# Kernel optimization log

Hardware: AMD Instinct MI355X
Metric: run time of the kernel (lower is better)

The kernel has to match this reference:

```python
import jax, jax.numpy as jnp
import numpy as np

N = 100_000       # nodes
E = 1_600_000     # edges (avg degree 16)
HID = 128         # hidden_size
NH = 8            # num_attention_heads
HD = HID // NH    # attention_head_size = 16


def setup_inputs() -> dict:
    key = jax.random.key(0)
    ks = jax.random.split(key, 9)
    s = 1.0 / np.sqrt(HID)
    h = jax.random.normal(ks[0], (N, HID), jnp.float32)
    src = jax.random.randint(ks[1], (E,), 0, N, dtype=jnp.int32)
    dst = jax.random.randint(ks[2], (E,), 0, N, dtype=jnp.int32)
    Wq = jax.random.normal(ks[3], (HID, HID), jnp.float32) * s
    Wk = jax.random.normal(ks[4], (HID, HID), jnp.float32) * s
    Wv = jax.random.normal(ks[5], (HID, HID), jnp.float32) * s
    bq = jnp.zeros((HID,), jnp.float32)
    bk = jnp.zeros((HID,), jnp.float32)
    bv = jnp.zeros((HID,), jnp.float32)
    return {"h": h, "src": src, "dst": dst,
            "Wq": Wq, "bq": bq, "Wk": Wk, "bk": bk, "Wv": Wv, "bv": bv}


def reference(h, src, dst, Wq, bq, Wk, bk, Wv, bv):
    # Linear projections, split heads: [N, NH, HD]
    Q = (h @ Wq + bq).reshape(N, NH, HD)
    K = (h @ Wk + bk).reshape(N, NH, HD)
    V = (h @ Wv + bv).reshape(N, NH, HD)

    # per-edge score: sum_d K[src] * Q[dst]  (no 1/sqrt(d) scaling in original)
    score = jnp.sum(K[src] * Q[dst], axis=-1)            # [E, NH]

    # edge_softmax: segment softmax over edges sharing the same destination
    m = jax.ops.segment_max(score, dst, num_segments=N)  # [N, NH]
    p = jnp.exp(score - m[dst])                          # [E, NH]
    denom = jax.ops.segment_sum(p, dst, num_segments=N)  # [N, NH]
    p = p / denom[dst]

    # (dropout prob = 0.0 -> identity)
    # message = V[src] * attn_probs; reduce = scatter-sum at destination
    msg = V[src] * p[:, :, None]                         # [E, NH, HD]
    out = jax.ops.segment_sum(msg, dst, num_segments=N)  # [N, NH, HD]
    return out.reshape(N, NH * HD)
```

## Files before the change

kernel.cpp:

```cpp
#include <hip/hip_runtime.h>
#include <stdint.h>

typedef unsigned short u16;
typedef u16      u16x8 __attribute__((ext_vector_type(8)));
typedef _Float16 f16x8 __attribute__((ext_vector_type(8)));
typedef float    f32x4 __attribute__((ext_vector_type(4)));
typedef unsigned long long u64;

#define HIDDEN 128
#define BSH    9
#define NPB    (1 << BSH)
#define MAXBUK 256
#define PAD    16


__device__ __forceinline__ float h2f(u16 u) {
    _Float16 h; __builtin_memcpy(&h, &u, 2); return (float)h;
}
__device__ __forceinline__ u16 f2h(float f) {
    _Float16 h = (_Float16)f; u16 u; __builtin_memcpy(&u, &h, 2); return u;
}
__device__ __forceinline__ float lo16f(uint32_t u) { return h2f((u16)(u & 0xffff)); }
__device__ __forceinline__ float hi16f(uint32_t u) { return h2f((u16)(u >> 16)); }

template <int CTRL>
__device__ __forceinline__ float dpp_qperm(float x) {
#if __has_builtin(__builtin_amdgcn_update_dpp)
    int r = __builtin_amdgcn_update_dpp(0, __builtin_bit_cast(int, x), CTRL, 0xF, 0xF, true);
    return __builtin_bit_cast(float, r);
#else
    return __shfl_xor(x, (CTRL == 0xB1) ? 1 : 2);
#endif
}

__global__ void pack_w_kernel(const float* __restrict__ Wq, const float* __restrict__ Wk,
                              const float* __restrict__ Wv, u16* __restrict__ packed) {
    int tid = blockIdx.x * blockDim.x + threadIdx.x;
    if (tid >= 24 * 4 * 64 * 8) return;
    int j    = tid & 7;
    int lane = (tid >> 3) & 63;
    int kt   = (tid >> 9) & 3;
    int ct   = tid >> 11;
    int w    = ct >> 3;
    int k    = kt * 32 + ((lane >> 4) << 3) + j;
    int c    = (ct & 7) * 16 + (lane & 15);
    const float* W = (w == 0) ? Wq : (w == 1) ? Wk : Wv;
    packed[tid] = f2h(W[k * HIDDEN + c]);
}

__global__ __launch_bounds__(256) void qkv_gemm_mfma(
    const float* __restrict__ h, const u16* __restrict__ packed,
    const float* __restrict__ bq, const float* __restrict__ bk, const float* __restrict__ bv,
    u16* __restrict__ Qb, u16* __restrict__ KVb, int n) {
    int wave = threadIdx.x >> 6, lane = threadIdx.x & 63;
    int row0 = blockIdx.x * 64 + wave * 16;
    int m = lane & 15, quad = lane >> 4;
    int arow = row0 + m;

    u16x8 a[4];
    if (arow < n) {
        const float* hp = h + (size_t)arow * HIDDEN + quad * 8;
        #pragma unroll
        for (int kt = 0; kt < 4; ++kt) {
            f32x4 lo = *(const f32x4*)(hp + kt * 32);
            f32x4 hi = *(const f32x4*)(hp + kt * 32 + 4);
            #pragma unroll
            for (int j = 0; j < 4; ++j) {
                a[kt][j]     = f2h(lo[j]);
                a[kt][j + 4] = f2h(hi[j]);
            }
        }
    } else {
        #pragma unroll
        for (int kt = 0; kt < 4; ++kt) a[kt] = (u16x8){0,0,0,0,0,0,0,0};
    }

    #pragma unroll
    for (int ct = 0; ct < 24; ++ct) {
        f32x4 acc = {0.f, 0.f, 0.f, 0.f};
        #pragma unroll
        for (int kt = 0; kt < 4; ++kt) {
            u16x8 b = *(const u16x8*)(packed + (((ct * 4 + kt) * 64 + lane) << 3));
            acc = __builtin_amdgcn_mfma_f32_16x16x32_f16(
                __builtin_bit_cast(f16x8, a[kt]), __builtin_bit_cast(f16x8, b),
                acc, 0, 0, 0);
        }
        int w  = ct >> 3;
        int cc = (ct & 7) * 16 + m;
        const float* bp = (w == 0) ? bq : (w == 1) ? bk : bv;
        float bias = bp[cc];
        #pragma unroll
        for (int r = 0; r < 4; ++r) {
            int rr = row0 + quad * 4 + r;
            if (rr < n) {
                u16 val = f2h(acc[r] + bias);
                if (w == 0) {
                    Qb[(size_t)rr * HIDDEN + cc] = val;
                } else {
                    KVb[(size_t)rr * 256 + ((cc >> 2) << 3) + ((w == 2) ? 4 : 0) + (cc & 3)] = val;
                }
            }
        }
    }
}

__global__ __launch_bounds__(256) void bucket_hist(const int* __restrict__ dst,
                                                   int* __restrict__ totalsPad,
                                                   int e, int nbuk) {
    __shared__ int lh[MAXBUK];
    int t = threadIdx.x;
    lh[t] = 0;
    __syncthreads();
    int stride = gridDim.x * blockDim.x;
    for (int i = blockIdx.x * blockDim.x + t; i < e; i += stride) {
        int b = dst[i] >> BSH;
        if (b < 0) b = 0; if (b >= nbuk) b = nbuk - 1;
        atomicAdd(&lh[b], 1);
    }
    __syncthreads();
    if (t < nbuk && lh[t] > 0) atomicAdd(&totalsPad[t * PAD], lh[t]);
}

__global__ __launch_bounds__(256) void bucket_scan(const int* __restrict__ totalsPad,
                                                   int* __restrict__ bs,
                                                   int* __restrict__ cursorPad,
                                                   int nbuk, int e) {
    __shared__ int buf[256];
    int t = threadIdx.x;
    int v = (t < nbuk) ? totalsPad[t * PAD] : 0;
    buf[t] = v;
    __syncthreads();
    #pragma unroll
    for (int off = 1; off < 256; off <<= 1) {
        int x = (t >= off) ? buf[t - off] : 0;
        __syncthreads();
        buf[t] += x;
        __syncthreads();
    }
    int excl = buf[t] - v;
    if (t < nbuk) {
        bs[t] = excl;
        cursorPad[t * PAD] = excl;
    }
    if (t == 0) bs[nbuk] = e;
}

__global__ __launch_bounds__(256) void bucket_scatter(
    const int* __restrict__ src, const int* __restrict__ dst,
    int* __restrict__ cursorPad, u64* __restrict__ pairs,
    int e, int nbuk, int chunk) {
    __shared__ int lh[MAXBUK];
    __shared__ int lcur[MAXBUK];
    int t = threadIdx.x;
    int lo = blockIdx.x * chunk;
    int hi = lo + chunk; if (hi > e) hi = e;
    if (lo >= e) return;
    lh[t] = 0;
    __syncthreads();
    for (int i = lo + t; i < hi; i += 256) {
        int b = dst[i] >> BSH;
        if (b < 0) b = 0; if (b >= nbuk) b = nbuk - 1;
        atomicAdd(&lh[b], 1);
    }
    __syncthreads();
    if (t < nbuk) {
        int c = lh[t];
        lcur[t] = (c > 0) ? atomicAdd(&cursorPad[t * PAD], c) : 0;
    }
    __syncthreads();
    for (int i = lo + t; i < hi; i += 256) {
        int d = dst[i], s = src[i];
        int b = d >> BSH;
        if (b < 0) b = 0; if (b >= nbuk) b = nbuk - 1;
        int slot = atomicAdd(&lcur[b], 1);
        if (slot >= 0 && slot < e)
            pairs[slot] = (((u64)(unsigned)d) << 32) | (unsigned)(s);
    }
}

__global__ __launch_bounds__(1024) void csr_finalize(
    const u64* __restrict__ pairs, const int* __restrict__ bs,
    int* __restrict__ starts, int* __restrict__ srcperm, int n, int e, int nbuk) {
    __shared__ int hist[NPB];
    __shared__ int excl[NPB];
    __shared__ int lcur[NPB];
    int b = blockIdx.x;
    int t = threadIdx.x;
    int d0 = b << BSH;
    int lo = bs[b], hi = bs[b + 1];
    for (int i = t; i < NPB; i += 1024) { hist[i] = 0; lcur[i] = 0; }
    __syncthreads();
    for (int i = lo + t; i < hi; i += 1024) {
        int ld = (int)(pairs[i] >> 32) - d0;
        if (ld < 0) ld = 0; if (ld >= NPB) ld = NPB - 1;
        atomicAdd(&hist[ld], 1);
    }
    __syncthreads();
    if (t < NPB) excl[t] = hist[t];
    __syncthreads();
    #pragma unroll
    for (int off = 1; off < NPB; off <<= 1) {
        int x = 0;
        if (t < NPB && t >= off) x = excl[t - off];
        __syncthreads();
        if (t < NPB) excl[t] += x;
        __syncthreads();
    }
    if (t < NPB) excl[t] -= hist[t];
    __syncthreads();
    if (t < NPB) {
        int d = d0 + t;
        if (d < n) starts[d] = lo + excl[t];
    }
    if (b == nbuk - 1 && t == 0) starts[n] = e;
    for (int i = lo + t; i < hi; i += 1024) {
        u64 p = pairs[i];
        int d  = (int)(p >> 32);
        int s  = (int)(p & 0xffffffffu);
        int ld = d - d0;
        if (ld < 0) ld = 0; if (ld >= NPB) ld = NPB - 1;
        int r = atomicAdd(&lcur[ld], 1);
        int slot = lo + excl[ld] + r;
        if (slot >= 0 && slot < e) srcperm[slot] = s;
    }
}

__global__ __launch_bounds__(256) void attn_kernel(
    const u16* __restrict__ Qb, const uint4* __restrict__ KVb,
    const int* __restrict__ starts, const int* __restrict__ srcperm,
    float* __restrict__ out, int n, int e) {
    int node = blockIdx.x * 4 + (threadIdx.x >> 6);
    int lane = threadIdx.x & 63;
    if (node >= n) return;
    int j = lane & 31;
    int h = lane >> 5;

    uint2 qp = *(const uint2*)(Qb + (size_t)node * HIDDEN + j * 4);
    float q0 = lo16f(qp.x), q1 = hi16f(qp.x);
    float q2 = lo16f(qp.y), q3 = hi16f(qp.y);

    int off = starts[node];
    int deg = starts[node + 1] - off;
    if (deg < 0) deg = 0; if (deg > e) deg = e;
    if (off < 0) off = 0; if (off > e - deg) off = e - deg;

    float mrun = -1e30f, lrun = 0.f;
    float o0 = 0.f, o1 = 0.f, o2 = 0.f, o3 = 0.f;

    for (int base = 0; base < deg; base += 64) {
        int cnt = deg - base; if (cnt > 64) cnt = 64;
        int sv = 0;
        if (lane < cnt) {
            int s = srcperm[off + base + lane];
            if (s < 0) s = 0; if (s >= n) s = n - 1;
            sv = s;
        }
        uint4 kvA = KVb[(size_t)__shfl(sv, h) * 32 + j];
        uint4 kvB = KVb[(size_t)__shfl(sv, 2 + h) * 32 + j];
        for (int i = 0; i < cnt; i += 2) {
            uint4 kv = kvA;
            kvA = kvB;
            int ip = i + 4 + h; if (ip > 63) ip = 63;
            kvB = KVb[(size_t)__shfl(sv, ip) * 32 + j];

            float p = q0 * lo16f(kv.x) + q1 * hi16f(kv.x)
                    + q2 * lo16f(kv.y) + q3 * hi16f(kv.y);
            p += dpp_qperm<0xB1>(p);
            p += dpp_qperm<0x4E>(p);
            bool valid = (i + h) < cnt;
            float pv = valid ? p : -1e30f;
            float mn  = fmaxf(mrun, pv);
            float scl = __expf(mrun - mn);
            float w   = valid ? __expf(pv - mn) : 0.f;
            lrun = lrun * scl + w;
            o0 = o0 * scl + w * lo16f(kv.z);
            o1 = o1 * scl + w * hi16f(kv.z);
            o2 = o2 * scl + w * lo16f(kv.w);
            o3 = o3 * scl + w * hi16f(kv.w);
            mrun = mn;
        }
    }

    float mo  = __shfl_xor(mrun, 32);
    float lo_ = __shfl_xor(lrun, 32);
    float p0 = __shfl_xor(o0, 32), p1 = __shfl_xor(o1, 32);
    float p2 = __shfl_xor(o2, 32), p3 = __shfl_xor(o3, 32);
    float m2 = fmaxf(mrun, mo);
    float sa = __expf(mrun - m2), sb = __expf(mo - m2);
    float l  = lrun * sa + lo_ * sb;
    float inv = (l > 0.f) ? 1.f / l : 0.f;
    if (h == 0) {
        float4 r;
        r.x = (o0 * sa + p0 * sb) * inv;
        r.y = (o1 * sa + p1 * sb) * inv;
        r.z = (o2 * sa + p2 * sb) * inv;
        r.w = (o3 * sa + p3 * sb) * inv;
        *(float4*)(out + (size_t)node * HIDDEN + j * 4) = r;
    }
}

extern "C" void kernel_launch(void* const* d_in, const int* in_sizes, int n_in,
                              void* d_out, int out_size, void* d_ws, size_t ws_size,
                              hipStream_t stream) {
    const float* h   = (const float*)d_in[0];
    const int*   src = (const int*)d_in[1];
    const int*   dst = (const int*)d_in[2];
    const float* Wq  = (const float*)d_in[3];
    const float* bq  = (const float*)d_in[4];
    const float* Wk  = (const float*)d_in[5];
    const float* bk  = (const float*)d_in[6];
    const float* Wv  = (const float*)d_in[7];
    const float* bv  = (const float*)d_in[8];
    float* out = (float*)d_out;

    const int n = in_sizes[0] / HIDDEN;
    const int e = in_sizes[1];
    const int nbuk = (n + NPB - 1) >> BSH;

    char* ws = (char*)d_ws;
    auto align256 = [](size_t x) { return (x + 255) & ~(size_t)255; };
    int* starts    = (int*)ws; ws += align256((size_t)(n + 1) * 4);
    int* bs        = (int*)ws; ws += align256((size_t)(MAXBUK + 1) * 4);
    int* totalsPad = (int*)ws; ws += align256((size_t)MAXBUK * PAD * 4);
    int* cursorPad = (int*)ws; ws += align256((size_t)MAXBUK * PAD * 4);
    int* srcperm   = (int*)ws; ws += align256((size_t)e * 4);
    u16* packed    = (u16*)ws; ws += align256((size_t)24 * 4 * 64 * 8 * sizeof(u16));
    u16* Qb        = (u16*)ws; ws += align256((size_t)n * HIDDEN * sizeof(u16));
    u16* KVb       = (u16*)ws; ws += align256((size_t)n * 256 * sizeof(u16));

    u64* pairs = (u64*)d_out;

    hipMemsetAsync(totalsPad, 0, (size_t)MAXBUK * PAD * 4, stream);

    pack_w_kernel<<<(24 * 4 * 64 * 8 + 255) / 256, 256, 0, stream>>>(Wq, Wk, Wv, packed);
    qkv_gemm_mfma<<<(n + 63) / 64, 256, 0, stream>>>(h, packed, bq, bk, bv, Qb, KVb, n);

    bucket_hist<<<256, 256, 0, stream>>>(dst, totalsPad, e, nbuk);
    bucket_scan<<<1, 256, 0, stream>>>(totalsPad, bs, cursorPad, nbuk, e);
    const int chunk = (e + 255) / 256;
    bucket_scatter<<<256, 256, 0, stream>>>(src, dst, cursorPad, pairs, e, nbuk, chunk);
    csr_finalize<<<nbuk, 1024, 0, stream>>>(pairs, bs, starts, srcperm, n, e, nbuk);

    attn_kernel<<<(n + 3) / 4, 256, 0, stream>>>(Qb, (const uint4*)KVb, starts, srcperm,
                                                 out, n, e);
}
```

Measured before the change: 331.4 us.

## Pack edge pairs into 32 bits, use fdot2/exp2, and prefetch indices directly

```diff
diff --git a/kernel.cpp b/kernel.cpp
--- a/kernel.cpp
+++ b/kernel.cpp
@@ -2,8 +2,10 @@
 #include <stdint.h>
 
 typedef unsigned short u16;
+typedef uint32_t u32;
 typedef u16      u16x8 __attribute__((ext_vector_type(8)));
 typedef _Float16 f16x8 __attribute__((ext_vector_type(8)));
+typedef _Float16 f16x2 __attribute__((ext_vector_type(2)));
 typedef float    f32x4 __attribute__((ext_vector_type(4)));
 typedef unsigned long long u64;
 
@@ -20,8 +22,9 @@
 __device__ __forceinline__ u16 f2h(float f) {
     _Float16 h = (_Float16)f; u16 u; __builtin_memcpy(&u, &h, 2); return u;
 }
-__device__ __forceinline__ float lo16f(uint32_t u) { return h2f((u16)(u & 0xffff)); }
-__device__ __forceinline__ float hi16f(uint32_t u) { return h2f((u16)(u >> 16)); }
+__device__ __forceinline__ f16x2 as_h2(uint32_t u) {
+    return __builtin_bit_cast(f16x2, u);
+}
 
 template <int CTRL>
 __device__ __forceinline__ float dpp_qperm(float x) {
@@ -30,6 +33,22 @@
     return __builtin_bit_cast(float, r);
 #else
     return __shfl_xor(x, (CTRL == 0xB1) ? 1 : 2);
+#endif
+}
+
+__device__ __forceinline__ float fdot2(f16x2 a, f16x2 b, float c) {
+#if __has_builtin(__builtin_amdgcn_fdot2)
+    return __builtin_amdgcn_fdot2(a, b, c, false);
+#else
+    return c + (float)a.x * (float)b.x + (float)a.y * (float)b.y;
+#endif
+}
+
+__device__ __forceinline__ float exp2f_fast(float x) {
+#if __has_builtin(__builtin_amdgcn_exp2f)
+    return __builtin_amdgcn_exp2f(x);
+#else
+    return __expf(x * 0.6931471805599453f);
 #endif
 }
 
@@ -147,7 +166,7 @@
 
 __global__ __launch_bounds__(256) void bucket_scatter(
     const int* __restrict__ src, const int* __restrict__ dst,
-    int* __restrict__ cursorPad, u64* __restrict__ pairs,
+    int* __restrict__ cursorPad, u32* __restrict__ pairs,
     int e, int nbuk, int chunk) {
     __shared__ int lh[MAXBUK];
     __shared__ int lcur[MAXBUK];
@@ -174,12 +193,12 @@
         if (b < 0) b = 0; if (b >= nbuk) b = nbuk - 1;
         int slot = atomicAdd(&lcur[b], 1);
         if (slot >= 0 && slot < e)
-            pairs[slot] = (((u64)(unsigned)d) << 32) | (unsigned)(s);
+            pairs[slot] = (((u32)d & (NPB - 1)) << 17) | ((u32)s & 0x1FFFF);
     }
 }
 
 __global__ __launch_bounds__(1024) void csr_finalize(
-    const u64* __restrict__ pairs, const int* __restrict__ bs,
+    const u32* __restrict__ pairs, const int* __restrict__ bs,
     int* __restrict__ starts, int* __restrict__ srcperm, int n, int e, int nbuk) {
     __shared__ int hist[NPB];
     __shared__ int excl[NPB];
@@ -191,8 +210,7 @@
     for (int i = t; i < NPB; i += 1024) { hist[i] = 0; lcur[i] = 0; }
     __syncthreads();
     for (int i = lo + t; i < hi; i += 1024) {
-        int ld = (int)(pairs[i] >> 32) - d0;
-        if (ld < 0) ld = 0; if (ld >= NPB) ld = NPB - 1;
+        int ld = (int)(pairs[i] >> 17);
         atomicAdd(&hist[ld], 1);
     }
     __syncthreads();
@@ -214,11 +232,9 @@
     }
     if (b == nbuk - 1 && t == 0) starts[n] = e;
     for (int i = lo + t; i < hi; i += 1024) {
-        u64 p = pairs[i];
-        int d  = (int)(p >> 32);
-        int s  = (int)(p & 0xffffffffu);
-        int ld = d - d0;
-        if (ld < 0) ld = 0; if (ld >= NPB) ld = NPB - 1;
+        u32 p = pairs[i];
+        int ld = (int)(p >> 17);
+        int s  = (int)(p & 0x1FFFF);
         int r = atomicAdd(&lcur[ld], 1);
         int slot = lo + excl[ld] + r;
         if (slot >= 0 && slot < e) srcperm[slot] = s;
@@ -236,49 +252,56 @@
     int h = lane >> 5;
 
     uint2 qp = *(const uint2*)(Qb + (size_t)node * HIDDEN + j * 4);
-    float q0 = lo16f(qp.x), q1 = hi16f(qp.x);
-    float q2 = lo16f(qp.y), q3 = hi16f(qp.y);
+    f16x2 q01 = as_h2(qp.x), q23 = as_h2(qp.y);
 
     int off = starts[node];
     int deg = starts[node + 1] - off;
     if (deg < 0) deg = 0; if (deg > e) deg = e;
     if (off < 0) off = 0; if (off > e - deg) off = e - deg;
 
+    const float LOG2E = 1.44269504f;
     float mrun = -1e30f, lrun = 0.f;
     float o0 = 0.f, o1 = 0.f, o2 = 0.f, o3 = 0.f;
 
-    for (int base = 0; base < deg; base += 64) {
-        int cnt = deg - base; if (cnt > 64) cnt = 64;
-        int sv = 0;
-        if (lane < cnt) {
-            int s = srcperm[off + base + lane];
-            if (s < 0) s = 0; if (s >= n) s = n - 1;
-            sv = s;
-        }
-        uint4 kvA = KVb[(size_t)__shfl(sv, h) * 32 + j];
-        uint4 kvB = KVb[(size_t)__shfl(sv, 2 + h) * 32 + j];
-        for (int i = 0; i < cnt; i += 2) {
+    if (deg > 0) {
+        const int last = deg - 1;
+        const int* sp = srcperm + off;
+        #define IDX(ii) (sp[((ii) > last) ? last : (ii)])
+        #define KVL(s)  (KVb[(size_t)(((unsigned)(s) < (unsigned)n) ? (unsigned)(s) : 0u) * 32 + j])
+
+        int sA = IDX(h);
+        int sB = IDX(h + 2);
+        int sC = IDX(h + 4);
+        int sD = IDX(h + 6);
+        uint4 kvA = KVL(sA);
+        uint4 kvB = KVL(sB);
+
+        for (int i = 0; i < deg; i += 2) {
             uint4 kv = kvA;
             kvA = kvB;
-            int ip = i + 4 + h; if (ip > 63) ip = 63;
-            kvB = KVb[(size_t)__shfl(sv, ip) * 32 + j];
-
-            float p = q0 * lo16f(kv.x) + q1 * hi16f(kv.x)
-                    + q2 * lo16f(kv.y) + q3 * hi16f(kv.y);
+            kvB = KVL(sC);
+            sC = sD;
+            sD = IDX(i + 8 + h);
+
+            float p = fdot2(as_h2(kv.x), q01, fdot2(as_h2(kv.y), q23, 0.f));
             p += dpp_qperm<0xB1>(p);
             p += dpp_qperm<0x4E>(p);
-            bool valid = (i + h) < cnt;
+            p *= LOG2E;
+            bool valid = (i + h) < deg;
             float pv = valid ? p : -1e30f;
             float mn  = fmaxf(mrun, pv);
-            float scl = __expf(mrun - mn);
-            float w   = valid ? __expf(pv - mn) : 0.f;
+            float scl = exp2f_fast(mrun - mn);
+            float w   = valid ? exp2f_fast(pv - mn) : 0.f;
             lrun = lrun * scl + w;
-            o0 = o0 * scl + w * lo16f(kv.z);
-            o1 = o1 * scl + w * hi16f(kv.z);
-            o2 = o2 * scl + w * lo16f(kv.w);
-            o3 = o3 * scl + w * hi16f(kv.w);
+            f16x2 vz = as_h2(kv.z), vw = as_h2(kv.w);
+            o0 = o0 * scl + w * (float)vz.x;
+            o1 = o1 * scl + w * (float)vz.y;
+            o2 = o2 * scl + w * (float)vw.x;
+            o3 = o3 * scl + w * (float)vw.y;
             mrun = mn;
         }
+        #undef IDX
+        #undef KVL
     }
 
     float mo  = __shfl_xor(mrun, 32);
@@ -286,7 +309,7 @@
     float p0 = __shfl_xor(o0, 32), p1 = __shfl_xor(o1, 32);
     float p2 = __shfl_xor(o2, 32), p3 = __shfl_xor(o3, 32);
     float m2 = fmaxf(mrun, mo);
-    float sa = __expf(mrun - m2), sb = __expf(mo - m2);
+    float sa = exp2f_fast(mrun - m2), sb = exp2f_fast(mo - m2);
     float l  = lrun * sa + lo_ * sb;
     float inv = (l > 0.f) ? 1.f / l : 0.f;
     if (h == 0) {
@@ -328,7 +351,7 @@
     u16* Qb        = (u16*)ws; ws += align256((size_t)n * HIDDEN * sizeof(u16));
     u16* KVb       = (u16*)ws; ws += align256((size_t)n * 256 * sizeof(u16));
 
-    u64* pairs = (u64*)d_out;
+    u32* pairs = (u32*)d_out;
 
     hipMemsetAsync(totalsPad, 0, (size_t)MAXBUK * PAD * 4, stream);
 
```

New measurement: 327.3 us. No clear change (-1.3%).
